# Optimization experiments

Measured on AMD Instinct MI355X. Metric: run time of the kernel, lower is better.

The kernel has to match this reference:

```python
import jax, jax.numpy as jnp
import numpy as np

D_MODEL = 1024
N_HEADS = 16
HEAD_DIM = D_MODEL // N_HEADS
B, T = 2, 2048


def _rotate_half(x):
    # Faithful to module's _apply_rotary: view (..., D//2, 2), pair -> (-x1, x0)
    xr = x.reshape(*x.shape[:-1], HEAD_DIM // 2, 2)
    rot = jnp.stack([-xr[..., 1], xr[..., 0]], axis=-1)
    return rot.reshape(*x.shape)


def setup_inputs() -> dict:
    key = jax.random.key(0)
    ks = jax.random.split(key, 9)
    s = 1.0 / np.sqrt(D_MODEL)
    return {
        "x": jax.random.normal(ks[0], (B, T, D_MODEL), jnp.float32),
        "Wq": jax.random.normal(ks[1], (D_MODEL, D_MODEL), jnp.float32) * s,
        "bq": jax.random.normal(ks[2], (D_MODEL,), jnp.float32) * 0.02,
        "Wk": jax.random.normal(ks[3], (D_MODEL, D_MODEL), jnp.float32) * s,
        "bk": jax.random.normal(ks[4], (D_MODEL,), jnp.float32) * 0.02,
        "Wv": jax.random.normal(ks[5], (D_MODEL, D_MODEL), jnp.float32) * s,
        "bv": jax.random.normal(ks[6], (D_MODEL,), jnp.float32) * 0.02,
        "Wo": jax.random.normal(ks[7], (D_MODEL, D_MODEL), jnp.float32) * s,
        "bo": jax.random.normal(ks[8], (D_MODEL,), jnp.float32) * 0.02,
    }


def reference(x, Wq, bq, Wk, bk, Wv, bv, Wo, bo):
    b, t, _ = x.shape
    # QKV projections (nn.Linear: x @ W.T + b), split heads -> (B, H, T, Dh)
    def proj(W, bias):
        y = x @ W.T + bias
        return y.reshape(b, t, N_HEADS, HEAD_DIM).transpose(0, 2, 1, 3)

    q = _rotate_half(proj(Wq, bq))
    k = _rotate_half(proj(Wk, bk))
    v = proj(Wv, bv)

    scale = 1.0 / jnp.sqrt(jnp.asarray(HEAD_DIM, x.dtype))
    scores = jnp.einsum('bhqd,bhkd->bhqk', q, k) * scale
    causal = jnp.tril(jnp.ones((t, t), bool))  # (T, T)
    scores = jnp.where(causal, scores, jnp.asarray(-jnp.inf, scores.dtype))
    attn = jax.nn.softmax(scores, axis=-1)
    out = jnp.einsum('bhqk,bhkd->bhqd', attn, v)
    out = out.transpose(0, 2, 1, 3).reshape(b, t, D_MODEL)
    return out @ Wo.T + bo
```

## Files before the change

kernel.cpp:

```cpp
#include <hip/hip_runtime.h>
#include <stdint.h>

#define DM 1024
#define NH 16
#define HD 64
#define BB 2
#define TT 2048
#define MT (BB*TT)

typedef __bf16 bfrag __attribute__((ext_vector_type(8)));
typedef float  f32x4 __attribute__((ext_vector_type(4)));

__device__ __forceinline__ unsigned short f2bf(float f) {
  union { float f; unsigned u; } v; v.f = f;
  unsigned r = v.u + 0x7fffu + ((v.u >> 16) & 1u);
  return (unsigned short)(r >> 16);
}

__device__ __forceinline__ unsigned short f2bf_hw(float f) {
  __bf16 b = (__bf16)f;
  union { __bf16 b; unsigned short u; } v; v.b = b;
  return v.u;
}

__device__ __forceinline__ unsigned int pack2bf(float a, float b) {
  union { __bf16 h[2]; unsigned int u; } v;
  v.h[0] = (__bf16)a; v.h[1] = (__bf16)b;
  return v.u;
}

__device__ __forceinline__ void async16(const void* g, void* l) {
  __builtin_amdgcn_global_load_lds(
      (const __attribute__((address_space(1))) unsigned int*)g,
      (__attribute__((address_space(3))) unsigned int*)l, 16, 0, 0);
}

#define CBAR() do { asm volatile("" ::: "memory"); \
                    __builtin_amdgcn_s_barrier();  \
                    asm volatile("" ::: "memory"); } while (0)

#define QSCALE 0.18033688011112043f
#define M2BIAS 15.869645449778597f

__global__ __launch_bounds__(256) void cvt_kernel(
    const float* __restrict__ x,  const float* __restrict__ Wq,
    const float* __restrict__ Wk, const float* __restrict__ Wv,
    const float* __restrict__ Wo,
    unsigned short* __restrict__ xb, unsigned short* __restrict__ wqkv,
    unsigned short* __restrict__ wob) {
  int i = blockIdx.x * 256 + threadIdx.x;
  const int NX = MT * DM / 4;
  const int NW = DM * DM / 4;
  const float* src; unsigned short* dst; int off;
  if      (i < NX)        { src = x;  dst = xb;              off = i; }
  else if (i < NX + NW)   { src = Wq; dst = wqkv;            off = i - NX; }
  else if (i < NX + 2*NW) { src = Wk; dst = wqkv + DM*DM;    off = i - NX - NW; }
  else if (i < NX + 3*NW) { src = Wv; dst = wqkv + 2*DM*DM;  off = i - NX - 2*NW; }
  else                    { src = Wo; dst = wob;             off = i - NX - 3*NW; }
  float4 v = ((const float4*)src)[off];
  ushort4 o;
  o.x = f2bf(v.x); o.y = f2bf(v.y); o.z = f2bf(v.z); o.w = f2bf(v.w);
  ((ushort4*)dst)[off] = o;
}

__global__ __launch_bounds__(512, 2) void gemm_qkv(
    const unsigned short* __restrict__ A, const unsigned short* __restrict__ Bm,
    const float* __restrict__ bias0, const float* __restrict__ bias1,
    const float* __restrict__ bias2,
    unsigned short* __restrict__ Qo, unsigned short* __restrict__ Ko,
    unsigned short* __restrict__ Vo) {
  const int tid = threadIdx.x;
  const int wave = tid >> 6, lane = tid & 63;
  const int lr = lane & 15, quad = lane >> 4;
  const int flat = blockIdx.x;
  const int s = (flat & 7) * 32 + (flat >> 3);
  const int m0 = (s & 15) * 256, n0 = (s >> 4) * 192;

  __shared__ __align__(16) unsigned short sA[2][2][256 * 32];
  __shared__ __align__(16) unsigned short sB[2][2][192 * 32];

  const f32x4 zero = {0.f, 0.f, 0.f, 0.f};
  f32x4 acc[4][6];
#pragma unroll
  for (int i = 0; i < 4; i++)
#pragma unroll
    for (int j = 0; j < 6; j++) acc[i][j] = zero;

  const int wm = (wave >> 1) * 64, wn = (wave & 1) * 96;

  auto stagePart = [&](int h) {
    if (h >= 64) return;
    const int ts = h >> 2, pi = h & 3;
    const int buf = ts & 1, hk = pi >> 1;
    const int k0 = ts * 64 + (hk << 5);
    if (pi & 1) {
      unsigned short* dst = &sB[buf][hk][0];
      {
        int fb = wave * 512;
        int fl = fb + lane * 8;
        int row = fl >> 5, c = (fl >> 3) & 3;
        async16(Bm + (size_t)(n0 + row) * 1024 + k0 + ((c ^ ((row >> 1) & 3)) << 3),
                dst + fb);
      }
      if (wave < 4) {
        int fb = 4096 + wave * 512;
        int fl = fb + lane * 8;
        int row = fl >> 5, c = (fl >> 3) & 3;
        async16(Bm + (size_t)(n0 + row) * 1024 + k0 + ((c ^ ((row >> 1) & 3)) << 3),
                dst + fb);
      }
    } else {
      unsigned short* dst = &sA[buf][hk][0];
#pragma unroll
      for (int rep = 0; rep < 2; ++rep) {
        int fb = rep * 4096 + wave * 512;
        int fl = fb + lane * 8;
        int row = fl >> 5, c = (fl >> 3) & 3;
        async16(A + (size_t)(m0 + row) * 1024 + k0 + ((c ^ ((row >> 1) & 3)) << 3),
                dst + fb);
      }
    }
  };

#pragma unroll
  for (int h = 0; h < 6; ++h) stagePart(h);
  asm volatile("s_waitcnt vmcnt(6)" ::: "memory");
  CBAR();

  bfrag af[4], bf[3];
#pragma unroll 1
  for (int t = 0; t < 16; ++t) {
    const int buf = t & 1;
    const int P0 = 4 * t;

    auto rdA = [&](int hk) {
#pragma unroll
      for (int i = 0; i < 4; i++) {
        int ra = wm + i * 16 + lr;
        af[i] = *(const bfrag*)&sA[buf][hk][ra * 32 + ((quad ^ ((ra >> 1) & 3)) << 3)];
      }
    };
    auto rdB = [&](int hk, int jh) {
#pragma unroll
      for (int jj = 0; jj < 3; jj++) {
        int rb = wn + (jh * 3 + jj) * 16 + lr;
        bf[jj] = *(const bfrag*)&sB[buf][hk][rb * 32 + ((quad ^ ((rb >> 1) & 3)) << 3)];
      }
    };
    auto domfma = [&](int jh) {
      __builtin_amdgcn_s_setprio(1);
#pragma unroll
      for (int i = 0; i < 4; i++)
#pragma unroll
        for (int jj = 0; jj < 3; jj++)
          acc[i][jh * 3 + jj] = __builtin_amdgcn_mfma_f32_16x16x32_bf16(
              af[i], bf[jj], acc[i][jh * 3 + jj], 0, 0, 0);
      __builtin_amdgcn_s_setprio(0);
    };

    rdA(0); rdB(0, 0);
    stagePart(P0 + 6);
    CBAR();
    domfma(0);
    rdB(0, 1);
    stagePart(P0 + 7);
    if (t == 15) { asm volatile("s_waitcnt vmcnt(0)" ::: "memory"); }
    else         { asm volatile("s_waitcnt vmcnt(6)" ::: "memory"); }
    CBAR();
    domfma(1);
    rdA(1); rdB(1, 0);
    stagePart(P0 + 8);
    CBAR();
    domfma(0);
    rdB(1, 1);
    stagePart(P0 + 9);
    if (t == 14)      { asm volatile("s_waitcnt vmcnt(3)" ::: "memory"); }
    else if (t < 14)  { asm volatile("s_waitcnt vmcnt(6)" ::: "memory"); }
    CBAR();
    domfma(1);
  }

#pragma unroll
  for (int j = 0; j < 6; j++) {
    int n = n0 + wn + j * 16 + lr;
    int qkv = n >> 10, nn = n & 1023;
    float bias = (qkv == 0 ? bias0 : qkv == 1 ? bias1 : bias2)[nn];
    int h = nn >> 6, d = nn & 63;
    if (qkv == 2) {
#pragma unroll
      for (int i = 0; i < 4; i++) {
        int t0 = m0 + wm + i * 16 + quad * 4;
        int b = t0 >> 11, tt = t0 & 2047;
        size_t bb = (size_t)((b << 4) + h) * (TT * 64);
        int kk0 = tt & 63;
        size_t off = bb + (size_t)(tt >> 6) * 4096 +
                     (size_t)((kk0 >> 3) << 9) + (d << 3) + (kk0 & 7);
        ushort4 pk;
        pk.x = f2bf(acc[i][j][0] + bias);
        pk.y = f2bf(acc[i][j][1] + bias);
        pk.z = f2bf(acc[i][j][2] + bias);
        pk.w = f2bf(acc[i][j][3] + bias);
        *(ushort4*)(Vo + off) = pk;
      }
    } else {
#pragma unroll
      for (int i = 0; i < 4; i++)
#pragma unroll
        for (int r = 0; r < 4; r++) {
          int m = m0 + wm + i * 16 + quad * 4 + r;
          float vb = acc[i][j][r] + bias;
          float pv = __shfl_xor(vb, 1);
          float val = (n & 1) ? pv : -pv;
          int b = m >> 11, t = m & 2047;
          size_t base = (size_t)((b << 4) + h) * (TT * 64);
          if (qkv == 0) {
            Qo[base + (size_t)t * 64 + d] = f2bf(val * QSCALE);
          } else {
            int kk = t & 63;
            size_t off = base + (size_t)(t >> 6) * 4096 +
                         (size_t)((d >> 3) << 9) + (kk << 3) + (d & 7);
            Ko[off] = f2bf(val);
          }
        }
    }
  }
}

__global__ __launch_bounds__(512, 2) void gemm_op(
    const unsigned short* __restrict__ A, const unsigned short* __restrict__ Bm,
    const float* __restrict__ bias0, float* __restrict__ Co) {
  const int tid = threadIdx.x;
  const int wave = tid >> 6, lane = tid & 63;
  const int lr = lane & 15, quad = lane >> 4;
  const int flat = blockIdx.x;
  const int s = (flat & 7) * 32 + (flat >> 3);
  const int m0 = (s >> 3) * 128, n0 = (s & 7) * 128;

  __shared__ __align__(16) unsigned short sA[2][2][128 * 32];
  __shared__ __align__(16) unsigned short sB[2][2][128 * 32];

  const f32x4 zero = {0.f, 0.f, 0.f, 0.f};
  f32x4 acc[4][2];
#pragma unroll
  for (int i = 0; i < 4; i++)
#pragma unroll
    for (int j = 0; j < 2; j++) acc[i][j] = zero;

  const int wm = (wave >> 2) * 64, wn = (wave & 3) * 32;

  auto stagePart = [&](int h) {
    if (h >= 32) return;
    const int ts = h >> 1, hk = h & 1;
    const int buf = ts & 1;
    const int k0 = ts * 64 + (hk << 5);
    int fb = wave * 512;
    int fl = fb + lane * 8;
    int row = fl >> 5, c = (fl >> 3) & 3;
    int col = (c ^ ((row >> 1) & 3)) << 3;
    async16(A  + (size_t)(m0 + row) * 1024 + k0 + col, &sA[buf][hk][fb]);
    async16(Bm + (size_t)(n0 + row) * 1024 + k0 + col, &sB[buf][hk][fb]);
  };

#pragma unroll
  for (int h = 0; h < 3; ++h) stagePart(h);
  asm volatile("s_waitcnt vmcnt(4)" ::: "memory");
  CBAR();

#pragma unroll 1
  for (int t = 0; t < 16; ++t) {
    const int buf = t & 1;
#pragma unroll
    for (int hk = 0; hk < 2; ++hk) {
      bfrag af[4], bfr[2];
#pragma unroll
      for (int i = 0; i < 4; i++) {
        int ra = wm + i * 16 + lr;
        af[i] = *(const bfrag*)&sA[buf][hk][ra * 32 + ((quad ^ ((ra >> 1) & 3)) << 3)];
      }
#pragma unroll
      for (int jj = 0; jj < 2; jj++) {
        int rb = wn + jj * 16 + lr;
        bfr[jj] = *(const bfrag*)&sB[buf][hk][rb * 32 + ((quad ^ ((rb >> 1) & 3)) << 3)];
      }
      stagePart(2 * t + hk + 3);
      if (hk == 0) {
        if (t < 15) { asm volatile("s_waitcnt vmcnt(4)" ::: "memory"); }
        else        { asm volatile("s_waitcnt vmcnt(0)" ::: "memory"); }
      } else {
        if (t < 14)       { asm volatile("s_waitcnt vmcnt(4)" ::: "memory"); }
        else if (t == 14) { asm volatile("s_waitcnt vmcnt(2)" ::: "memory"); }
      }
      CBAR();
      __builtin_amdgcn_s_setprio(1);
#pragma unroll
      for (int i = 0; i < 4; i++)
#pragma unroll
        for (int jj = 0; jj < 2; jj++)
          acc[i][jj] = __builtin_amdgcn_mfma_f32_16x16x32_bf16(
              af[i], bfr[jj], acc[i][jj], 0, 0, 0);
      __builtin_amdgcn_s_setprio(0);
    }
  }

#pragma unroll
  for (int j = 0; j < 2; j++) {
    int n = n0 + wn + j * 16 + lr;
    float bias = bias0[n];
#pragma unroll
    for (int i = 0; i < 4; i++)
#pragma unroll
      for (int r = 0; r < 4; r++) {
        int m = m0 + wm + i * 16 + quad * 4 + r;
        Co[(size_t)m * 1024 + n] = acc[i][j][r] + bias;
      }
  }
}

__global__ __launch_bounds__(256, 4) void flash_kernel(
    const unsigned short* __restrict__ Qg, const unsigned short* __restrict__ Kg,
    const unsigned short* __restrict__ Vg, unsigned short* __restrict__ Og) {
  const int flat = blockIdx.x;
  const int xcd = flat & 7;
  const int idx = flat >> 3;
  const int g   = idx >> 5;
  const int bh  = g * 8 + xcd;
  const int a   = idx & 31;
  const int qt  = (g & 1) ? (31 - a) : a;
  const int tid = threadIdx.x, wave = tid >> 6, lane = tid & 63;
  const int lr = lane & 15, quad = lane >> 4;
  __shared__ __align__(16) unsigned short sP[4][1024];
  const size_t base = (size_t)bh * (TT * 64);
  const int nS = qt + 1;
  const int qg = qt * 64 + wave * 16 + lr;
  const f32x4 zero = {0.f, 0.f, 0.f, 0.f};

  bfrag qf0, qf1;
  {
    const unsigned short* qr = Qg + base + (size_t)qg * 64;
    qf0 = *(const bfrag*)(qr + quad * 8);
    qf1 = *(const bfrag*)(qr + 32 + quad * 8);
  }
  f32x4 o[4];
  float rs = 0.f;
#pragma unroll
  for (int j = 0; j < 4; j++) o[j] = zero;

  const unsigned short* kgb = Kg + base;
  const unsigned short* vgb = Vg + base;
  const int lko = quad * 512 + lr * 8;

  const int pwr = lr * 8 + (quad & 1) * 4;
  const int pq2 = quad >> 1;

#pragma unroll 1
  for (int kt = 0; kt < nS; ++kt) {
    const unsigned short* kt_k = kgb + (size_t)kt * 4096;
    const unsigned short* kt_v = vgb + (size_t)kt * 4096;
    bfrag kf0[4], kf1[4], vf0[4], vf1[4];
#pragma unroll
    for (int ct = 0; ct < 4; ct++) {
      kf0[ct] = *(const bfrag*)(kt_k + lko + ct * 128);
      kf1[ct] = *(const bfrag*)(kt_k + 2048 + lko + ct * 128);
    }
#pragma unroll
    for (int j = 0; j < 4; j++) {
      vf0[j] = *(const bfrag*)(kt_v + lko + j * 128);
      vf1[j] = *(const bfrag*)(kt_v + 2048 + lko + j * 128);
    }
    f32x4 sT[4];
    __builtin_amdgcn_s_setprio(1);
#pragma unroll
    for (int ct = 0; ct < 4; ct++) {
      f32x4 t = __builtin_amdgcn_mfma_f32_16x16x32_bf16(kf0[ct], qf0, zero, 0, 0, 0);
      sT[ct]  = __builtin_amdgcn_mfma_f32_16x16x32_bf16(kf1[ct], qf1, t,    0, 0, 0);
    }
    __builtin_amdgcn_s_setprio(0);
    const bool diag = (kt == qt);
#pragma unroll
    for (int ct = 0; ct < 4; ++ct) {
      float e[4];
#pragma unroll
      for (int r = 0; r < 4; ++r)
        e[r] = exp2f(sT[ct][r] - M2BIAS);
      if (diag) {
#pragma unroll
        for (int r = 0; r < 4; ++r) {
          int key = kt * 64 + ct * 16 + quad * 4 + r;
          if (key > qg) e[r] = 0.f;
        }
      }
      rs += (e[0] + e[1]) + (e[2] + e[3]);
      uint2 w;
      w.x = pack2bf(e[0], e[1]);
      w.y = pack2bf(e[2], e[3]);
      *(uint2*)&sP[wave][(ct * 2 + pq2) * 128 + pwr] = w;
    }
    bfrag pf0 = *(const bfrag*)&sP[wave][quad * 128 + lr * 8];
    bfrag pf1 = *(const bfrag*)&sP[wave][(4 + quad) * 128 + lr * 8];
    __builtin_amdgcn_s_setprio(1);
#pragma unroll
    for (int j = 0; j < 4; j++) {
      o[j] = __builtin_amdgcn_mfma_f32_16x16x32_bf16(vf0[j], pf0, o[j], 0, 0, 0);
      o[j] = __builtin_amdgcn_mfma_f32_16x16x32_bf16(vf1[j], pf1, o[j], 0, 0, 0);
    }
    __builtin_amdgcn_s_setprio(0);
  }

  rs += __shfl_xor(rs, 16); rs += __shfl_xor(rs, 32);
  const float inv = 1.0f / rs;

  const int b = bh >> 4, h = bh & 15;
#pragma unroll
  for (int j = 0; j < 4; j++) {
    ushort4 pk;
    pk.x = f2bf_hw(o[j][0] * inv); pk.y = f2bf_hw(o[j][1] * inv);
    pk.z = f2bf_hw(o[j][2] * inv); pk.w = f2bf_hw(o[j][3] * inv);
    int col = h * 64 + j * 16 + quad * 4;
    *(ushort4*)(Og + (size_t)(b * TT + qg) * 1024 + col) = pk;
  }
}

extern "C" void kernel_launch(void* const* d_in, const int* in_sizes, int n_in,
                              void* d_out, int out_size, void* d_ws, size_t ws_size,
                              hipStream_t stream) {
  const float* x  = (const float*)d_in[0];
  const float* Wq = (const float*)d_in[1];
  const float* bq = (const float*)d_in[2];
  const float* Wk = (const float*)d_in[3];
  const float* bk = (const float*)d_in[4];
  const float* Wv = (const float*)d_in[5];
  const float* bv = (const float*)d_in[6];
  const float* Wo = (const float*)d_in[7];
  const float* bo = (const float*)d_in[8];
  float* out = (float*)d_out;

  unsigned short* ws = (unsigned short*)d_ws;
  unsigned short* xb   = ws;
  unsigned short* wqkv = ws + (size_t)4 * 1024 * 1024;
  unsigned short* wob  = ws + (size_t)7 * 1024 * 1024;
  unsigned short* Qb   = ws + (size_t)8 * 1024 * 1024;
  unsigned short* Kb   = ws + (size_t)12 * 1024 * 1024;
  unsigned short* Vb   = ws + (size_t)16 * 1024 * 1024;
  unsigned short* Ob   = ws + (size_t)20 * 1024 * 1024;

  cvt_kernel<<<dim3(8192), dim3(256), 0, stream>>>(x, Wq, Wk, Wv, Wo, xb, wqkv, wob);
  gemm_qkv<<<dim3(256), dim3(512), 0, stream>>>(xb, wqkv, bq, bk, bv, Qb, Kb, Vb);
  flash_kernel<<<dim3(1024), dim3(256), 0, stream>>>(Qb, Kb, Vb, Ob);
  gemm_op<<<dim3(256), dim3(512), 0, stream>>>(Ob, wob, bo, out);
}
```

Baseline: 183.2 us.

## Process two KV tiles per flash iteration with dual accumulators

The flash attention loop now handles two 64-key tiles per iteration. All K/V fragments for both tiles are loaded up front and pinned in registers, and the work uses separate output and row-sum accumulators that are merged at the end. This is meant to expose more memory-level parallelism and more independent MFMA chains per wave. In exchange, launch bounds drop occupancy to 2 blocks per SIMD, the P staging buffer in shared memory doubles, and the query-tile ordering becomes uniformly longest-first. Register pressure rises substantially, and fewer resident waves may hide less latency.

Result: slower. 205.5 us (+12.2%).

```diff
diff --git a/kernel.cpp b/kernel.cpp
--- a/kernel.cpp
+++ b/kernel.cpp
@@ -38,6 +38,8 @@
 #define CBAR() do { asm volatile("" ::: "memory"); \
                     __builtin_amdgcn_s_barrier();  \
                     asm volatile("" ::: "memory"); } while (0)
+
+#define PIN(x) asm volatile("" : "+v"(x))
 
 #define QSCALE 0.18033688011112043f
 #define M2BIAS 15.869645449778597f
@@ -316,7 +318,7 @@
   }
 }
 
-__global__ __launch_bounds__(256, 4) void flash_kernel(
+__global__ __launch_bounds__(256, 2) void flash_kernel(
     const unsigned short* __restrict__ Qg, const unsigned short* __restrict__ Kg,
     const unsigned short* __restrict__ Vg, unsigned short* __restrict__ Og) {
   const int flat = blockIdx.x;
@@ -324,11 +326,10 @@
   const int idx = flat >> 3;
   const int g   = idx >> 5;
   const int bh  = g * 8 + xcd;
-  const int a   = idx & 31;
-  const int qt  = (g & 1) ? (31 - a) : a;
+  const int qt  = 31 - (idx & 31);
   const int tid = threadIdx.x, wave = tid >> 6, lane = tid & 63;
   const int lr = lane & 15, quad = lane >> 4;
-  __shared__ __align__(16) unsigned short sP[4][1024];
+  __shared__ __align__(16) unsigned short sP[4][2048];
   const size_t base = (size_t)bh * (TT * 64);
   const int nS = qt + 1;
   const int qg = qt * 64 + wave * 16 + lr;
@@ -340,10 +341,10 @@
     qf0 = *(const bfrag*)(qr + quad * 8);
     qf1 = *(const bfrag*)(qr + 32 + quad * 8);
   }
-  f32x4 o[4];
-  float rs = 0.f;
-#pragma unroll
-  for (int j = 0; j < 4; j++) o[j] = zero;
+  f32x4 oA[4], oB[4];
+  float rsA = 0.f, rsB = 0.f;
+#pragma unroll
+  for (int j = 0; j < 4; j++) { oA[j] = zero; oB[j] = zero; }
 
   const unsigned short* kgb = Kg + base;
   const unsigned short* vgb = Vg + base;
@@ -351,70 +352,139 @@
 
   const int pwr = lr * 8 + (quad & 1) * 4;
   const int pq2 = quad >> 1;
+  const int npair = (nS + 1) >> 1;
 
 #pragma unroll 1
-  for (int kt = 0; kt < nS; ++kt) {
-    const unsigned short* kt_k = kgb + (size_t)kt * 4096;
-    const unsigned short* kt_v = vgb + (size_t)kt * 4096;
-    bfrag kf0[4], kf1[4], vf0[4], vf1[4];
+  for (int ip = 0; ip < npair; ++ip) {
+    const int ka = 2 * ip, kb = ka + 1;
+    const bool hasB = (kb < nS);
+    const unsigned short* ak = kgb + (size_t)ka * 4096;
+    const unsigned short* av = vgb + (size_t)ka * 4096;
+    const unsigned short* bk = kgb + (size_t)kb * 4096;
+    const unsigned short* bv = vgb + (size_t)kb * 4096;
+
+    bfrag kA0[4], kA1[4], vA0[4], vA1[4];
+    bfrag kB0[4], kB1[4], vB0[4], vB1[4];
 #pragma unroll
     for (int ct = 0; ct < 4; ct++) {
-      kf0[ct] = *(const bfrag*)(kt_k + lko + ct * 128);
-      kf1[ct] = *(const bfrag*)(kt_k + 2048 + lko + ct * 128);
-    }
-#pragma unroll
-    for (int j = 0; j < 4; j++) {
-      vf0[j] = *(const bfrag*)(kt_v + lko + j * 128);
-      vf1[j] = *(const bfrag*)(kt_v + 2048 + lko + j * 128);
-    }
-    f32x4 sT[4];
+      kA0[ct] = *(const bfrag*)(ak + lko + ct * 128);
+      kA1[ct] = *(const bfrag*)(ak + 2048 + lko + ct * 128);
+      vA0[ct] = *(const bfrag*)(av + lko + ct * 128);
+      vA1[ct] = *(const bfrag*)(av + 2048 + lko + ct * 128);
+    }
+    if (hasB) {
+#pragma unroll
+      for (int ct = 0; ct < 4; ct++) {
+        kB0[ct] = *(const bfrag*)(bk + lko + ct * 128);
+        kB1[ct] = *(const bfrag*)(bk + 2048 + lko + ct * 128);
+        vB0[ct] = *(const bfrag*)(bv + lko + ct * 128);
+        vB1[ct] = *(const bfrag*)(bv + 2048 + lko + ct * 128);
+      }
+    }
+#pragma unroll
+    for (int ct = 0; ct < 4; ct++) {
+      PIN(kA0[ct]); PIN(kA1[ct]); PIN(vA0[ct]); PIN(vA1[ct]);
+    }
+    if (hasB) {
+#pragma unroll
+      for (int ct = 0; ct < 4; ct++) {
+        PIN(kB0[ct]); PIN(kB1[ct]); PIN(vB0[ct]); PIN(vB1[ct]);
+      }
+    }
+
+    f32x4 sTa[4], sTb[4];
     __builtin_amdgcn_s_setprio(1);
 #pragma unroll
     for (int ct = 0; ct < 4; ct++) {
-      f32x4 t = __builtin_amdgcn_mfma_f32_16x16x32_bf16(kf0[ct], qf0, zero, 0, 0, 0);
-      sT[ct]  = __builtin_amdgcn_mfma_f32_16x16x32_bf16(kf1[ct], qf1, t,    0, 0, 0);
+      f32x4 t = __builtin_amdgcn_mfma_f32_16x16x32_bf16(kA0[ct], qf0, zero, 0, 0, 0);
+      sTa[ct] = __builtin_amdgcn_mfma_f32_16x16x32_bf16(kA1[ct], qf1, t,    0, 0, 0);
+    }
+    if (hasB) {
+#pragma unroll
+      for (int ct = 0; ct < 4; ct++) {
+        f32x4 t = __builtin_amdgcn_mfma_f32_16x16x32_bf16(kB0[ct], qf0, zero, 0, 0, 0);
+        sTb[ct] = __builtin_amdgcn_mfma_f32_16x16x32_bf16(kB1[ct], qf1, t,    0, 0, 0);
+      }
     }
     __builtin_amdgcn_s_setprio(0);
-    const bool diag = (kt == qt);
+
+    const bool diagA = (ka == qt), diagB = (kb == qt);
 #pragma unroll
     for (int ct = 0; ct < 4; ++ct) {
       float e[4];
 #pragma unroll
       for (int r = 0; r < 4; ++r)
-        e[r] = exp2f(sT[ct][r] - M2BIAS);
-      if (diag) {
+        e[r] = exp2f(sTa[ct][r] - M2BIAS);
+      if (diagA) {
 #pragma unroll
         for (int r = 0; r < 4; ++r) {
-          int key = kt * 64 + ct * 16 + quad * 4 + r;
+          int key = ka * 64 + ct * 16 + quad * 4 + r;
           if (key > qg) e[r] = 0.f;
         }
       }
-      rs += (e[0] + e[1]) + (e[2] + e[3]);
+      rsA += (e[0] + e[1]) + (e[2] + e[3]);
       uint2 w;
       w.x = pack2bf(e[0], e[1]);
       w.y = pack2bf(e[2], e[3]);
       *(uint2*)&sP[wave][(ct * 2 + pq2) * 128 + pwr] = w;
     }
-    bfrag pf0 = *(const bfrag*)&sP[wave][quad * 128 + lr * 8];
-    bfrag pf1 = *(const bfrag*)&sP[wave][(4 + quad) * 128 + lr * 8];
+    if (hasB) {
+#pragma unroll
+      for (int ct = 0; ct < 4; ++ct) {
+        float e[4];
+#pragma unroll
+        for (int r = 0; r < 4; ++r)
+          e[r] = exp2f(sTb[ct][r] - M2BIAS);
+        if (diagB) {
+#pragma unroll
+          for (int r = 0; r < 4; ++r) {
+            int key = kb * 64 + ct * 16 + quad * 4 + r;
+            if (key > qg) e[r] = 0.f;
+          }
+        }
+        rsB += (e[0] + e[1]) + (e[2] + e[3]);
+        uint2 w;
+        w.x = pack2bf(e[0], e[1]);
+        w.y = pack2bf(e[2], e[3]);
+        *(uint2*)&sP[wave][1024 + (ct * 2 + pq2) * 128 + pwr] = w;
+      }
+    }
+
+    bfrag pfa0 = *(const bfrag*)&sP[wave][quad * 128 + lr * 8];
+    bfrag pfa1 = *(const bfrag*)&sP[wave][(4 + quad) * 128 + lr * 8];
+    bfrag pfb0, pfb1;
+    if (hasB) {
+      pfb0 = *(const bfrag*)&sP[wave][1024 + quad * 128 + lr * 8];
+      pfb1 = *(const bfrag*)&sP[wave][1024 + (4 + quad) * 128 + lr * 8];
+    }
+
     __builtin_amdgcn_s_setprio(1);
 #pragma unroll
     for (int j = 0; j < 4; j++) {
-      o[j] = __builtin_amdgcn_mfma_f32_16x16x32_bf16(vf0[j], pf0, o[j], 0, 0, 0);
-      o[j] = __builtin_amdgcn_mfma_f32_16x16x32_bf16(vf1[j], pf1, o[j], 0, 0, 0);
+      oA[j] = __builtin_amdgcn_mfma_f32_16x16x32_bf16(vA0[j], pfa0, oA[j], 0, 0, 0);
+      oA[j] = __builtin_amdgcn_mfma_f32_16x16x32_bf16(vA1[j], pfa1, oA[j], 0, 0, 0);
+    }
+    if (hasB) {
+#pragma unroll
+      for (int j = 0; j < 4; j++) {
+        oB[j] = __builtin_amdgcn_mfma_f32_16x16x32_bf16(vB0[j], pfb0, oB[j], 0, 0, 0);
+        oB[j] = __builtin_amdgcn_mfma_f32_16x16x32_bf16(vB1[j], pfb1, oB[j], 0, 0, 0);
+      }
     }
     __builtin_amdgcn_s_setprio(0);
   }
 
+  float rs = rsA + rsB;
   rs += __shfl_xor(rs, 16); rs += __shfl_xor(rs, 32);
   const float inv = 1.0f / rs;
 
   const int b = bh >> 4, h = bh & 15;
 #pragma unroll
   for (int j = 0; j < 4; j++) {
+    f32x4 o = oA[j] + oB[j];
     ushort4 pk;
-    pk.x = f2bf_hw(o[j][0] * inv); pk.y = f2bf_hw(o[j][1] * inv);
-    pk.z = f2bf_hw(o[j][2] * inv); pk.w = f2bf_hw(o[j][3] * inv);
+    pk.x = f2bf_hw(o[0] * inv); pk.y = f2bf_hw(o[1] * inv);
+    pk.z = f2bf_hw(o[2] * inv); pk.w = f2bf_hw(o[3] * inv);
     int col = h * 64 + j * 16 + quad * 4;
     *(ushort4*)(Og + (size_t)(b * TT + qg) * 1024 + col) = pk;
   }
```

## Double-buffer K/V register fragments in flash attention loop

Applied to the files above, without the earlier changes.

Restructures the flash attention key-tile loop to prefetch the next tile's K and V fragments into a second register set while computing the current tile, unrolled by two with sched_barriers to keep loads ahead of MFMAs. This targets global load latency exposed at the start of each iteration. To fit the doubled fragment registers, launch bounds are relaxed from 4 to 2 blocks per CU, which may reduce occupancy and latency hiding across waves.

New measurement: 193.2 us. 1.05x slower.

```diff
diff --git a/kernel.cpp b/kernel.cpp
--- a/kernel.cpp
+++ b/kernel.cpp
@@ -316,7 +316,7 @@
   }
 }
 
-__global__ __launch_bounds__(256, 4) void flash_kernel(
+__global__ __launch_bounds__(256, 2) void flash_kernel(
     const unsigned short* __restrict__ Qg, const unsigned short* __restrict__ Kg,
     const unsigned short* __restrict__ Vg, unsigned short* __restrict__ Og) {
   const int flat = blockIdx.x;
@@ -352,27 +352,28 @@
   const int pwr = lr * 8 + (quad & 1) * 4;
   const int pq2 = quad >> 1;
 
-#pragma unroll 1
-  for (int kt = 0; kt < nS; ++kt) {
-    const unsigned short* kt_k = kgb + (size_t)kt * 4096;
-    const unsigned short* kt_v = vgb + (size_t)kt * 4096;
-    bfrag kf0[4], kf1[4], vf0[4], vf1[4];
+  bfrag kA0[4], kA1[4], vA0[4], vA1[4];
+  bfrag kB0[4], kB1[4], vB0[4], vB1[4];
+
+  auto loadT = [&](bfrag k0[4], bfrag k1[4], bfrag v0[4], bfrag v1[4], int kt) {
+    const unsigned short* tk = kgb + (size_t)kt * 4096;
+    const unsigned short* tv = vgb + (size_t)kt * 4096;
 #pragma unroll
     for (int ct = 0; ct < 4; ct++) {
-      kf0[ct] = *(const bfrag*)(kt_k + lko + ct * 128);
-      kf1[ct] = *(const bfrag*)(kt_k + 2048 + lko + ct * 128);
-    }
-#pragma unroll
-    for (int j = 0; j < 4; j++) {
-      vf0[j] = *(const bfrag*)(kt_v + lko + j * 128);
-      vf1[j] = *(const bfrag*)(kt_v + 2048 + lko + j * 128);
-    }
+      k0[ct] = *(const bfrag*)(tk + lko + ct * 128);
+      k1[ct] = *(const bfrag*)(tk + 2048 + lko + ct * 128);
+      v0[ct] = *(const bfrag*)(tv + lko + ct * 128);
+      v1[ct] = *(const bfrag*)(tv + 2048 + lko + ct * 128);
+    }
+  };
+
+  auto computeT = [&](bfrag k0[4], bfrag k1[4], bfrag v0[4], bfrag v1[4], int kt) {
     f32x4 sT[4];
     __builtin_amdgcn_s_setprio(1);
 #pragma unroll
     for (int ct = 0; ct < 4; ct++) {
-      f32x4 t = __builtin_amdgcn_mfma_f32_16x16x32_bf16(kf0[ct], qf0, zero, 0, 0, 0);
-      sT[ct]  = __builtin_amdgcn_mfma_f32_16x16x32_bf16(kf1[ct], qf1, t,    0, 0, 0);
+      f32x4 t = __builtin_amdgcn_mfma_f32_16x16x32_bf16(k0[ct], qf0, zero, 0, 0, 0);
+      sT[ct]  = __builtin_amdgcn_mfma_f32_16x16x32_bf16(k1[ct], qf1, t,    0, 0, 0);
     }
     __builtin_amdgcn_s_setprio(0);
     const bool diag = (kt == qt);
@@ -400,10 +401,24 @@
     __builtin_amdgcn_s_setprio(1);
 #pragma unroll
     for (int j = 0; j < 4; j++) {
-      o[j] = __builtin_amdgcn_mfma_f32_16x16x32_bf16(vf0[j], pf0, o[j], 0, 0, 0);
-      o[j] = __builtin_amdgcn_mfma_f32_16x16x32_bf16(vf1[j], pf1, o[j], 0, 0, 0);
+      o[j] = __builtin_amdgcn_mfma_f32_16x16x32_bf16(v0[j], pf0, o[j], 0, 0, 0);
+      o[j] = __builtin_amdgcn_mfma_f32_16x16x32_bf16(v1[j], pf1, o[j], 0, 0, 0);
     }
     __builtin_amdgcn_s_setprio(0);
+  };
+
+  loadT(kA0, kA1, vA0, vA1, 0);
+
+#pragma unroll 1
+  for (int kt = 0; kt < nS; kt += 2) {
+    if (kt + 1 < nS) loadT(kB0, kB1, vB0, vB1, kt + 1);
+    __builtin_amdgcn_sched_barrier(0);
+    computeT(kA0, kA1, vA0, vA1, kt);
+    if (kt + 1 < nS) {
+      if (kt + 2 < nS) loadT(kA0, kA1, vA0, vA1, kt + 2);
+      __builtin_amdgcn_sched_barrier(0);
+      computeT(kB0, kB1, vB0, vB1, kt + 1);
+    }
   }
 
   rs += __shfl_xor(rs, 16); rs += __shfl_xor(rs, 32);
```
